# Kernel tuning notes

Hardware: AMD Instinct MI355X
Metric: run time of the kernel (lower is better)

## Reference

```python
import jax, jax.numpy as jnp
import numpy as np

B, S, D, H, F = 16, 512, 1024, 16, 4096
DH = D // H
LN_EPS = 1e-12


def layer_norm(x, g, b):
    mu = jnp.mean(x, axis=-1, keepdims=True)
    var = jnp.mean(jnp.square(x - mu), axis=-1, keepdims=True)
    return (x - mu) * jax.lax.rsqrt(var + LN_EPS) * g + b


def setup_inputs() -> dict:
    key = jax.random.key(0)
    ks = jax.random.split(key, 16)
    s_attn = 1.0 / np.sqrt(D)
    s_ffn = 1.0 / np.sqrt(F)
    return {
        "hidden_states": jax.random.normal(ks[0], (B, S, D), jnp.float32),
        "attention_mask": jnp.zeros((B, S), jnp.float32),
        # weights stored [in, out]
        "Wq": jax.random.normal(ks[1], (D, D), jnp.float32) * s_attn,
        "bq": jnp.zeros((D,), jnp.float32),
        "Wk": jax.random.normal(ks[2], (D, D), jnp.float32) * s_attn,
        "bk": jnp.zeros((D,), jnp.float32),
        "Wv": jax.random.normal(ks[3], (D, D), jnp.float32) * s_attn,
        "bv": jnp.zeros((D,), jnp.float32),
        "Wo": jax.random.normal(ks[4], (D, D), jnp.float32) * s_attn,
        "bo": jnp.zeros((D,), jnp.float32),
        "ln1_g": jnp.ones((D,), jnp.float32),
        "ln1_b": jnp.zeros((D,), jnp.float32),
        "Wi": jax.random.normal(ks[5], (D, F), jnp.float32) * s_attn,
        "bi": jnp.zeros((F,), jnp.float32),
        "Wo2": jax.random.normal(ks[6], (F, D), jnp.float32) * s_ffn,
        "bo2": jnp.zeros((D,), jnp.float32),
        "ln2_g": jnp.ones((D,), jnp.float32),
        "ln2_b": jnp.zeros((D,), jnp.float32),
    }


def reference(hidden_states, attention_mask, Wq, bq, Wk, bk, Wv, bv, Wo, bo,
              ln1_g, ln1_b, Wi, bi, Wo2, bo2, ln2_g, ln2_b):
    x = hidden_states
    # --- self attention ---
    q = (x @ Wq + bq).reshape(B, S, H, DH)
    k = (x @ Wk + bk).reshape(B, S, H, DH)
    v = (x @ Wv + bv).reshape(B, S, H, DH)
    scores = jnp.einsum("bqhd,bkhd->bhqk", q, k) / np.sqrt(DH)
    scores = scores + attention_mask[:, None, None, :]
    probs = jax.nn.softmax(scores, axis=-1)  # dropout p=0 (eval)
    ctx = jnp.einsum("bhqk,bkhd->bqhd", probs, v).reshape(B, S, D)
    # --- self output: dense + residual + LN ---
    attn_out = layer_norm(ctx @ Wo + bo + x, ln1_g, ln1_b)
    # --- intermediate: dense + gelu (exact erf gelu, BERT) ---
    inter = jax.nn.gelu(attn_out @ Wi + bi, approximate=False)
    # --- output: dense + residual + LN ---
    out = layer_norm(inter @ Wo2 + bo2 + attn_out, ln2_g, ln2_b)
    return out
```

## Files before the change

kernel.cpp:

```cpp
#include <hip/hip_runtime.h>
#include <hip/hip_bf16.h>
#include <math.h>

#define DEV_INLINE __device__ __forceinline__

typedef __attribute__((ext_vector_type(8))) short bf16x8;
typedef __attribute__((ext_vector_type(8))) unsigned short u16x8;
typedef __attribute__((ext_vector_type(4))) float f32x4;


DEV_INLINE void gload_lds16(const void* g, void* l) {
  __builtin_amdgcn_global_load_lds(
      (__attribute__((address_space(1))) unsigned int*)const_cast<void*>(g),
      (__attribute__((address_space(3))) unsigned int*)l,
      16, 0, 0);
}

DEV_INLINE unsigned lds_a(const void* p) {
  return (unsigned)(unsigned long long)(__attribute__((address_space(3))) const void*)p;
}

DEV_INLINE short f2bs(float x) {
  union { __hip_bfloat16 h; short s; } u;
  u.h = __float2bfloat16(x);
  return u.s;
}

DEV_INLINE float bs2f(unsigned short s) {
  union { float f; unsigned u; } v;
  v.u = ((unsigned)s) << 16;
  return v.f;
}

DEV_INLINE f32x4 mfma16(bf16x8 a, bf16x8 b, f32x4 c) {
  return __builtin_amdgcn_mfma_f32_16x16x32_bf16(a, b, c, 0, 0, 0);
}

#define DSREAD_O(dst, base, imm) \
  asm volatile("ds_read_b128 %0, %1 offset:%2" : "=v"(dst) : "v"(base), "n"(imm))


__global__ __launch_bounds__(256)
void prep_all(const float* __restrict__ X, __hip_bfloat16* __restrict__ Xb,
              const float* __restrict__ Wq, const float* __restrict__ Wk,
              const float* __restrict__ Wv, const float* __restrict__ Wo,
              const float* __restrict__ Wi, const float* __restrict__ Wo2,
              __hip_bfloat16* __restrict__ WqkvT, __hip_bfloat16* __restrict__ WoT,
              __hip_bfloat16* __restrict__ WiT, __hip_bfloat16* __restrict__ Wo2T,
              const float* __restrict__ bq, const float* __restrict__ bk,
              const float* __restrict__ bv, float* __restrict__ bqkv)
{
  int bx = blockIdx.x;
  const int tid = threadIdx.x;

  if (bx < 8192) {
    const size_t i = ((size_t)bx * 256 + tid) * 4;
    const float4 x = *(const float4*)(X + i);
    union { __hip_bfloat16 h[4]; ushort4 u; } pk;
    pk.h[0] = __float2bfloat16(x.x);
    pk.h[1] = __float2bfloat16(x.y);
    pk.h[2] = __float2bfloat16(x.z);
    pk.h[3] = __float2bfloat16(x.w);
    *(ushort4*)(Xb + i) = pk.u;
    return;
  }
  bx -= 8192;
  if (bx < 4) {
    const int i = bx * 256 + tid;
    bqkv[i] = bq[i]; bqkv[1024 + i] = bk[i]; bqkv[2048 + i] = bv[i];
    return;
  }
  bx -= 4;

  const float* Wsrc; __hip_bfloat16* Wdst; int K, N, nt, kt;
  if (bx < 1024)      { Wsrc = Wq;  Wdst = WqkvT;               K = 1024; N = 1024; nt = bx & 31;  kt = bx >> 5; }
  else if (bx < 2048) { const int l = bx - 1024; Wsrc = Wk;  Wdst = WqkvT + 1024 * 1024; K = 1024; N = 1024; nt = l & 31;  kt = l >> 5; }
  else if (bx < 3072) { const int l = bx - 2048; Wsrc = Wv;  Wdst = WqkvT + 2048 * 1024; K = 1024; N = 1024; nt = l & 31;  kt = l >> 5; }
  else if (bx < 4096) { const int l = bx - 3072; Wsrc = Wo;  Wdst = WoT;  K = 1024; N = 1024; nt = l & 31;  kt = l >> 5; }
  else if (bx < 8192) { const int l = bx - 4096; Wsrc = Wi;  Wdst = WiT;  K = 1024; N = 4096; nt = l & 127; kt = l >> 7; }
  else                { const int l = bx - 8192; Wsrc = Wo2; Wdst = Wo2T; K = 4096; N = 1024; nt = l & 31;  kt = l >> 5; }

  __shared__ float t[32][33];
  const int n0 = nt * 32, k0 = kt * 32;
  const int tx = tid & 31, ty = tid >> 5;
#pragma unroll
  for (int r = ty; r < 32; r += 8)
    t[r][tx] = Wsrc[(size_t)(k0 + r) * N + n0 + tx];
  __syncthreads();
#pragma unroll
  for (int r = ty; r < 32; r += 8)
    Wdst[(size_t)(n0 + r) * K + k0 + tx] = __float2bfloat16(t[tx][r]);
}


template<int MODE>
DEV_INLINE void gemm256_body(const short* __restrict__ A, const short* __restrict__ Bt,
                             const float* __restrict__ bias,
                             __hip_bfloat16* __restrict__ Cb,
                             int M, int N, int K)
{
  __shared__ __align__(128) short lds[24576];

  const int tid = threadIdx.x;
  const int lane = tid & 63, wid = tid >> 6;
  const int q4 = lane >> 4, c16 = lane & 15;
  const int wm = (wid >> 1) * 64, wn = (wid & 1) * 64;

  const int nNT = N >> 7;
  int bid = blockIdx.x;
  { const int cpx = (int)gridDim.x >> 3; bid = (bid & 7) * cpx + (bid >> 3); }
  const int bm = (bid / nNT) * 256;
  const int bn = (bid % nNT) * 128;

  const int sr = tid >> 3, sl = tid & 7;
  const int sg = (sl ^ (sr & 7)) * 8;
  const short* pA = A  + (size_t)(bm + sr) * K + sg;
  const short* pB = Bt + (size_t)(bn + sr) * K + sg;
  char* const baseA = (char*)lds;
  char* const baseB = (char*)lds + 32768;

  f32x4 acc[4][4];
#pragma unroll
  for (int i = 0; i < 4; ++i)
#pragma unroll
    for (int j = 0; j < 4; ++j) acc[i][j] = (f32x4){0.f, 0.f, 0.f, 0.f};

  for (int kt = 0; kt < K; kt += 64) {
    __syncthreads();
#pragma unroll
    for (int u = 0; u < 4; ++u)
      gload_lds16(pA + (size_t)u * 64 * K + kt, baseA + u * 8192 + wid * 1024);
#pragma unroll
    for (int u = 0; u < 2; ++u)
      gload_lds16(pB + (size_t)u * 64 * K + kt, baseB + u * 8192 + wid * 1024);
    __syncthreads();

#pragma unroll
    for (int kk = 0; kk < 2; ++kk) {
      bf16x8 af[4], bfr[4];
#pragma unroll
      for (int mt = 0; mt < 4; ++mt)
        af[mt] = *(const bf16x8*)(baseA + (wm + mt * 16 + c16) * 128 +
                                  (((kk * 4 + q4) ^ (c16 & 7)) * 16));
#pragma unroll
      for (int nt = 0; nt < 4; ++nt)
        bfr[nt] = *(const bf16x8*)(baseB + (wn + nt * 16 + c16) * 128 +
                                   (((kk * 4 + q4) ^ (c16 & 7)) * 16));
#pragma unroll
      for (int mt = 0; mt < 4; ++mt)
#pragma unroll
        for (int nt = 0; nt < 4; ++nt)
          acc[mt][nt] = mfma16(af[mt], bfr[nt], acc[mt][nt]);
    }
  }

  __syncthreads();

  float* eb = (float*)((char*)lds + wid * 4352);
  const int erow = lane >> 2, ecol = (lane & 3) * 16;
#pragma unroll
  for (int mf = 0; mf < 4; ++mf) {
#pragma unroll
    for (int nf = 0; nf < 4; ++nf) {
      const int col = bn + wn + nf * 16 + c16;
      const float bsv = bias[col];
#pragma unroll
      for (int j = 0; j < 4; ++j) {
        float v = acc[mf][nf][j] + bsv;
        if constexpr (MODE == 2)
          v = 0.5f * v * (1.0f + erff(v * 0.70710678118654752f));
        eb[(q4 * 4 + j) * 68 + nf * 16 + c16] = v;
      }
    }
    const int gr = bm + wm + mf * 16 + erow;
    const size_t gbase = (size_t)gr * N + bn + wn + ecol;
    unsigned short* cp = (unsigned short*)Cb;
#pragma unroll
    for (int u = 0; u < 2; ++u) {
      float4 a = *(float4*)&eb[erow * 68 + ecol + u * 8];
      float4 b = *(float4*)&eb[erow * 68 + ecol + u * 8 + 4];
      u16x8 o;
      o[0] = (unsigned short)f2bs(a.x); o[1] = (unsigned short)f2bs(a.y);
      o[2] = (unsigned short)f2bs(a.z); o[3] = (unsigned short)f2bs(a.w);
      o[4] = (unsigned short)f2bs(b.x); o[5] = (unsigned short)f2bs(b.y);
      o[6] = (unsigned short)f2bs(b.z); o[7] = (unsigned short)f2bs(b.w);
      *(u16x8*)(cp + gbase + u * 8) = o;
    }
  }
}


template<int MODE>
DEV_INLINE void gemm64_body(const short* __restrict__ A, const short* __restrict__ Bt,
                            const float* __restrict__ bias,
                            const float* __restrict__ residf,
                            const unsigned short* __restrict__ residb,
                            __hip_bfloat16* __restrict__ Cb,
                            int M, int N, int K)
{
  __shared__ __align__(128) short lds[32768];

  const int tid = threadIdx.x;
  const int lane = tid & 63, w = tid >> 6;
  const int q4 = lane >> 4, c16 = lane & 15;
  const int wm = (w >> 1) * 64, wn = (w & 1) * 64;

  const int nNT = N >> 7;
  int bid = blockIdx.x;
  { const int cpx = (int)gridDim.x >> 3; bid = (bid & 7) * cpx + (bid >> 3); }
  const int bm = (bid / nNT) * 128;
  const int bn = (bid % nNT) * 128;

  const int sr = tid >> 3, sl = tid & 7;
  const int sg = (sl ^ (sr & 7)) * 8;
  const short* pA = A  + (size_t)(bm + sr) * K + sg;
  const short* pB = Bt + (size_t)(bn + sr) * K + sg;

  const int s0 = (q4 ^ (c16 & 7)) * 16;
  const int s1 = ((q4 ^ 4) ^ (c16 & 7)) * 16;
  unsigned aRd0 = lds_a(lds) + (unsigned)((wm + c16) * 128 + s0);
  unsigned aRd1 = lds_a(lds) + (unsigned)((wm + c16) * 128 + s1);
  unsigned bRd0 = lds_a(lds) + (unsigned)(16384 + (wn + c16) * 128 + s0);
  unsigned bRd1 = lds_a(lds) + (unsigned)(16384 + (wn + c16) * 128 + s1);

  f32x4 acc[4][4];
#pragma unroll
  for (int i = 0; i < 4; ++i)
#pragma unroll
    for (int j = 0; j < 4; ++j) acc[i][j] = (f32x4){0.f, 0.f, 0.f, 0.f};

  auto stage = [&](int buf, int kt) {
    char* b = (char*)lds + buf * 32768;
#pragma unroll
    for (int u = 0; u < 4; ++u) {
      gload_lds16(pA + (size_t)u * 32 * K + kt, b + u * 4096 + w * 1024);
      gload_lds16(pB + (size_t)u * 32 * K + kt, b + 16384 + u * 4096 + w * 1024);
    }
  };

  stage(0, 0);
  __syncthreads();

  const int NT = K >> 6;
  int cur = 0;
  for (int t = 0; t < NT; ++t) {
    __builtin_amdgcn_sched_barrier(0);
    if (t + 1 < NT) stage(cur ^ 1, (t + 1) << 6);
    __builtin_amdgcn_sched_barrier(0);

    bf16x8 a0, a1, a2, a3, a4, a5, a6, a7;
    bf16x8 b0, b1, b2, b3, b4, b5, b6, b7;
    DSREAD_O(a0, aRd0, 0 * 2048); DSREAD_O(a1, aRd0, 1 * 2048);
    DSREAD_O(a2, aRd0, 2 * 2048); DSREAD_O(a3, aRd0, 3 * 2048);
    DSREAD_O(b0, bRd0, 0 * 2048); DSREAD_O(b1, bRd0, 1 * 2048);
    DSREAD_O(b2, bRd0, 2 * 2048); DSREAD_O(b3, bRd0, 3 * 2048);
    DSREAD_O(a4, aRd1, 0 * 2048); DSREAD_O(a5, aRd1, 1 * 2048);
    DSREAD_O(a6, aRd1, 2 * 2048); DSREAD_O(a7, aRd1, 3 * 2048);
    DSREAD_O(b4, bRd1, 0 * 2048); DSREAD_O(b5, bRd1, 1 * 2048);
    DSREAD_O(b6, bRd1, 2 * 2048); DSREAD_O(b7, bRd1, 3 * 2048);

    asm volatile("s_waitcnt lgkmcnt(0)");
    __builtin_amdgcn_sched_barrier(0);
    __builtin_amdgcn_s_setprio(1);
    acc[0][0] = mfma16(a0, b0, acc[0][0]); acc[0][1] = mfma16(a0, b1, acc[0][1]);
    acc[0][2] = mfma16(a0, b2, acc[0][2]); acc[0][3] = mfma16(a0, b3, acc[0][3]);
    acc[1][0] = mfma16(a1, b0, acc[1][0]); acc[1][1] = mfma16(a1, b1, acc[1][1]);
    acc[1][2] = mfma16(a1, b2, acc[1][2]); acc[1][3] = mfma16(a1, b3, acc[1][3]);
    acc[2][0] = mfma16(a2, b0, acc[2][0]); acc[2][1] = mfma16(a2, b1, acc[2][1]);
    acc[2][2] = mfma16(a2, b2, acc[2][2]); acc[2][3] = mfma16(a2, b3, acc[2][3]);
    acc[3][0] = mfma16(a3, b0, acc[3][0]); acc[3][1] = mfma16(a3, b1, acc[3][1]);
    acc[3][2] = mfma16(a3, b2, acc[3][2]); acc[3][3] = mfma16(a3, b3, acc[3][3]);
    acc[0][0] = mfma16(a4, b4, acc[0][0]); acc[0][1] = mfma16(a4, b5, acc[0][1]);
    acc[0][2] = mfma16(a4, b6, acc[0][2]); acc[0][3] = mfma16(a4, b7, acc[0][3]);
    acc[1][0] = mfma16(a5, b4, acc[1][0]); acc[1][1] = mfma16(a5, b5, acc[1][1]);
    acc[1][2] = mfma16(a5, b6, acc[1][2]); acc[1][3] = mfma16(a5, b7, acc[1][3]);
    acc[2][0] = mfma16(a6, b4, acc[2][0]); acc[2][1] = mfma16(a6, b5, acc[2][1]);
    acc[2][2] = mfma16(a6, b6, acc[2][2]); acc[2][3] = mfma16(a6, b7, acc[2][3]);
    acc[3][0] = mfma16(a7, b4, acc[3][0]); acc[3][1] = mfma16(a7, b5, acc[3][1]);
    acc[3][2] = mfma16(a7, b6, acc[3][2]); acc[3][3] = mfma16(a7, b7, acc[3][3]);
    __builtin_amdgcn_s_setprio(0);

    __syncthreads();
    aRd0 ^= 0x8000; aRd1 ^= 0x8000; bRd0 ^= 0x8000; bRd1 ^= 0x8000; cur ^= 1;
  }

  float* eb = (float*)((char*)lds + w * 4352);
  const int erow = lane >> 2, ecol = (lane & 3) * 16;
#pragma unroll
  for (int mf = 0; mf < 4; ++mf) {
#pragma unroll
    for (int nf = 0; nf < 4; ++nf) {
      const int col = bn + wn + nf * 16 + c16;
      const float bsv = bias[col];
#pragma unroll
      for (int j = 0; j < 4; ++j)
        eb[(q4 * 4 + j) * 68 + nf * 16 + c16] = acc[mf][nf][j] + bsv;
    }
    const int gr = bm + wm + mf * 16 + erow;
    const size_t gbase = (size_t)gr * N + bn + wn + ecol;
    unsigned short* cp = (unsigned short*)Cb;
#pragma unroll
    for (int u = 0; u < 2; ++u) {
      float4 a = *(float4*)&eb[erow * 68 + ecol + u * 8];
      float4 b = *(float4*)&eb[erow * 68 + ecol + u * 8 + 4];
      if constexpr (MODE == 3) {
        const float4 ra = *(const float4*)&residf[gbase + u * 8];
        const float4 rb = *(const float4*)&residf[gbase + u * 8 + 4];
        a.x += ra.x; a.y += ra.y; a.z += ra.z; a.w += ra.w;
        b.x += rb.x; b.y += rb.y; b.z += rb.z; b.w += rb.w;
      } else {
        const u16x8 rv = *(const u16x8*)(residb + gbase + u * 8);
        a.x += bs2f(rv[0]); a.y += bs2f(rv[1]); a.z += bs2f(rv[2]); a.w += bs2f(rv[3]);
        b.x += bs2f(rv[4]); b.y += bs2f(rv[5]); b.z += bs2f(rv[6]); b.w += bs2f(rv[7]);
      }
      u16x8 o;
      o[0] = (unsigned short)f2bs(a.x); o[1] = (unsigned short)f2bs(a.y);
      o[2] = (unsigned short)f2bs(a.z); o[3] = (unsigned short)f2bs(a.w);
      o[4] = (unsigned short)f2bs(b.x); o[5] = (unsigned short)f2bs(b.y);
      o[6] = (unsigned short)f2bs(b.z); o[7] = (unsigned short)f2bs(b.w);
      *(u16x8*)(cp + gbase + u * 8) = o;
    }
  }
}

__global__ __launch_bounds__(512)
void gemm_qkv(const short* A, const short* Bt, const float* bias,
              __hip_bfloat16* Cb, int M, int N, int K) {
  gemm256_body<0>(A, Bt, bias, Cb, M, N, K);
}
__global__ __launch_bounds__(512)
void gemm_wi(const short* A, const short* Bt, const float* bias,
             __hip_bfloat16* Cb, int M, int N, int K) {
  gemm256_body<2>(A, Bt, bias, Cb, M, N, K);
}
__global__ __launch_bounds__(256)
void gemm_wo(const short* A, const short* Bt, const float* bias,
             const float* residf, __hip_bfloat16* Cb, int M, int N, int K) {
  gemm64_body<3>(A, Bt, bias, residf, nullptr, Cb, M, N, K);
}
__global__ __launch_bounds__(256)
void gemm_wo2(const short* A, const short* Bt, const float* bias,
              const unsigned short* residb, __hip_bfloat16* Cb, int M, int N, int K) {
  gemm64_body<4>(A, Bt, bias, nullptr, residb, Cb, M, N, K);
}


__global__ __launch_bounds__(256)
void attn_flash(const short* __restrict__ Q, const short* __restrict__ Kmat,
                const short* __restrict__ V, const float* __restrict__ mask,
                __hip_bfloat16* __restrict__ ctx, int qs)
{
  __shared__ short Ksm[64 * 64];
  __shared__ short Vsm[64 * 64];
  __shared__ short Psm[4 * 16 * 64];

  const int tid = threadIdx.x;
  const int lane = tid & 63;
  const int w = tid >> 6;
  const int q4 = lane >> 4;
  const int c16 = lane & 15;
  const int b = blockIdx.z;
  const int h = blockIdx.y;
  const int qb = blockIdx.x;

  const size_t rowbase = (size_t)b * 512;
  const int hoff = h * 64;

  bf16x8 aq[2];
  {
    const size_t qrow = rowbase + (size_t)qb * 64 + w * 16 + c16;
    const short* qp = Q + qrow * qs + hoff + q4 * 8;
    aq[0] = *(const bf16x8*)(qp);
    aq[1] = *(const bf16x8*)(qp + 32);
  }

  float m_r[4], l_r[4];
  f32x4 O[4];
#pragma unroll
  for (int j = 0; j < 4; ++j) { m_r[j] = -INFINITY; l_r[j] = 0.f; O[j] = (f32x4){0.f, 0.f, 0.f, 0.f}; }

  const int kc0 = w * 128 + lane;
  const int kp0 = kc0 >> 3, kd0 = (kc0 & 7) * 8;
  const int kc1 = kc0 + 64;
  const int kp1 = kc1 >> 3, kd1 = (kc1 & 7) * 8;

  for (int kv0 = 0; kv0 < 512; kv0 += 64) {
    __syncthreads();
    gload_lds16(Kmat + (rowbase + kv0 + kp0) * qs + hoff + (kd0 ^ ((kp0 & 7) << 3)),
                (char*)Ksm + (size_t)(w * 128 + 0) * 16);
    gload_lds16(Kmat + (rowbase + kv0 + kp1) * qs + hoff + (kd1 ^ ((kp1 & 7) << 3)),
                (char*)Ksm + (size_t)(w * 128 + 64) * 16);
#pragma unroll
    for (int it = 0; it < 2; ++it) {
      const int c = tid + 256 * it;
      const int kp = c >> 3;
      const int dh8 = (c & 7) * 8;
      const bf16x8 vv = *(const bf16x8*)(V + (rowbase + kv0 + kp) * qs + hoff + dh8);
#pragma unroll
      for (int j = 0; j < 8; ++j) {
        const int dh = dh8 + j;
        *(short*)((char*)Vsm + dh * 128 + ((kp * 2) ^ ((dh & 7) << 4))) = vv[j];
      }
    }
    __syncthreads();

    float pv[4][4];
    float mk[4];
#pragma unroll
    for (int t = 0; t < 4; ++t) mk[t] = mask[rowbase + kv0 + t * 16 + c16];
#pragma unroll
    for (int t = 0; t < 4; ++t) {
      f32x4 z = (f32x4){0.f, 0.f, 0.f, 0.f};
      const int kp = t * 16 + c16;
#pragma unroll
      for (int ks = 0; ks < 2; ++ks) {
        const int d = ks * 32 + q4 * 8;
        bf16x8 kf = *(const bf16x8*)((char*)Ksm + kp * 128 + ((d * 2) ^ ((kp & 7) << 4)));
        z = mfma16(aq[ks], kf, z);
      }
#pragma unroll
      for (int j = 0; j < 4; ++j) pv[t][j] = z[j] * 0.125f + mk[t];
    }

#pragma unroll
    for (int j = 0; j < 4; ++j) {
      float mt_ = fmaxf(fmaxf(pv[0][j], pv[1][j]), fmaxf(pv[2][j], pv[3][j]));
#pragma unroll
      for (int o = 8; o >= 1; o >>= 1) mt_ = fmaxf(mt_, __shfl_xor(mt_, o));
      const float mn = fmaxf(m_r[j], mt_);
      const float sc = __expf(m_r[j] - mn);
      float rs = 0.f;
#pragma unroll
      for (int t = 0; t < 4; ++t) { const float pe = __expf(pv[t][j] - mn); pv[t][j] = pe; rs += pe; }
#pragma unroll
      for (int o = 8; o >= 1; o >>= 1) rs += __shfl_xor(rs, o);
      l_r[j] = l_r[j] * sc + rs;
      m_r[j] = mn;
#pragma unroll
      for (int nt = 0; nt < 4; ++nt) O[nt][j] *= sc;
    }

    char* pb = (char*)Psm + w * 2048;
#pragma unroll
    for (int j = 0; j < 4; ++j) {
      const int r = q4 * 4 + j;
#pragma unroll
      for (int t = 0; t < 4; ++t) {
        const int ck = t * 16 + c16;
        *(short*)(pb + r * 128 + ((ck * 2) ^ ((r & 7) << 4))) = f2bs(pv[t][j]);
      }
    }

#pragma unroll
    for (int ks = 0; ks < 2; ++ks) {
      const int kk = ks * 32 + q4 * 8;
      bf16x8 pa = *(const bf16x8*)(pb + c16 * 128 + ((kk * 2) ^ ((c16 & 7) << 4)));
#pragma unroll
      for (int nt = 0; nt < 4; ++nt) {
        const int dh = nt * 16 + c16;
        bf16x8 vf = *(const bf16x8*)((char*)Vsm + dh * 128 + ((kk * 2) ^ ((dh & 7) << 4)));
        O[nt] = mfma16(pa, vf, O[nt]);
      }
    }
  }

  float rinv[4];
#pragma unroll
  for (int j = 0; j < 4; ++j) rinv[j] = 1.0f / l_r[j];
#pragma unroll
  for (int nt = 0; nt < 4; ++nt) {
#pragma unroll
    for (int j = 0; j < 4; ++j) {
      const size_t row = rowbase + (size_t)qb * 64 + w * 16 + q4 * 4 + j;
      ctx[row * 1024 + hoff + nt * 16 + c16] = __float2bfloat16(O[nt][j] * rinv[j]);
    }
  }
}


template<int OUTB>
DEV_INLINE void ln_body(const unsigned short* __restrict__ in, const float* __restrict__ gam,
                        const float* __restrict__ bet, float* __restrict__ outf,
                        unsigned short* __restrict__ outb)
{
  const int row = blockIdx.x;
  const int tid = threadIdx.x;
  const size_t base = (size_t)row * 1024 + tid * 4;
  const ushort4 xi = *(const ushort4*)(in + base);
  const float x0 = bs2f(xi.x), x1 = bs2f(xi.y), x2 = bs2f(xi.z), x3 = bs2f(xi.w);
  float s  = x0 + x1 + x2 + x3;
  float s2 = x0 * x0 + x1 * x1 + x2 * x2 + x3 * x3;
#pragma unroll
  for (int o = 32; o >= 1; o >>= 1) { s += __shfl_xor(s, o); s2 += __shfl_xor(s2, o); }
  __shared__ float sb[8];
  const int w = tid >> 6;
  if ((tid & 63) == 0) { sb[w] = s; sb[w + 4] = s2; }
  __syncthreads();
  const float ts  = sb[0] + sb[1] + sb[2] + sb[3];
  const float ts2 = sb[4] + sb[5] + sb[6] + sb[7];
  const float mu = ts * (1.0f / 1024.0f);
  const float var = ts2 * (1.0f / 1024.0f) - mu * mu;
  const float rstd = rsqrtf(var + 1e-12f);
  const float4 g4 = *(const float4*)(gam + tid * 4);
  const float4 b4 = *(const float4*)(bet + tid * 4);
  const float y0 = (x0 - mu) * rstd * g4.x + b4.x;
  const float y1 = (x1 - mu) * rstd * g4.y + b4.y;
  const float y2 = (x2 - mu) * rstd * g4.z + b4.z;
  const float y3 = (x3 - mu) * rstd * g4.w + b4.w;
  if constexpr (OUTB) {
    ushort4 o;
    o.x = (unsigned short)f2bs(y0); o.y = (unsigned short)f2bs(y1);
    o.z = (unsigned short)f2bs(y2); o.w = (unsigned short)f2bs(y3);
    *(ushort4*)(outb + base) = o;
  } else {
    float4 y; y.x = y0; y.y = y1; y.z = y2; y.w = y3;
    *(float4*)(outf + base) = y;
  }
}

__global__ __launch_bounds__(256)
void ln_attn(const unsigned short* in, const float* gam, const float* bet,
             unsigned short* outb) { ln_body<1>(in, gam, bet, nullptr, outb); }
__global__ __launch_bounds__(256)
void ln_ffn(const unsigned short* in, const float* gam, const float* bet, float* outf) {
  ln_body<0>(in, gam, bet, outf, nullptr);
}


extern "C" void kernel_launch(void* const* d_in, const int* in_sizes, int n_in,
                              void* d_out, int out_size, void* d_ws, size_t ws_size,
                              hipStream_t stream)
{
  const float* X    = (const float*)d_in[0];
  const float* mask = (const float*)d_in[1];
  const float* Wq   = (const float*)d_in[2];   const float* bq  = (const float*)d_in[3];
  const float* Wk   = (const float*)d_in[4];   const float* bk  = (const float*)d_in[5];
  const float* Wv   = (const float*)d_in[6];   const float* bv  = (const float*)d_in[7];
  const float* Wo   = (const float*)d_in[8];   const float* bo  = (const float*)d_in[9];
  const float* g1   = (const float*)d_in[10];  const float* b1  = (const float*)d_in[11];
  const float* Wi   = (const float*)d_in[12];  const float* bi  = (const float*)d_in[13];
  const float* Wo2  = (const float*)d_in[14];  const float* bo2 = (const float*)d_in[15];
  const float* g2   = (const float*)d_in[16];  const float* b2  = (const float*)d_in[17];
  float* out = (float*)d_out;
  (void)in_sizes; (void)n_in; (void)out_size; (void)ws_size;

  const size_t D = 1024, F = 4096;
  const size_t MN = 8192 * D;

  char* p = (char*)d_ws;
  auto alloc = [&](size_t bytes) { char* r = p; p += (bytes + 255) & ~(size_t)255; return r; };
  short* Xb    = (short*)alloc(MN * 2);
  short* QKVb  = (short*)alloc(8192 * 3072 * 2);
  short* WqkvT = (short*)alloc(3072 * D * 2);
  short* WoT   = (short*)alloc(D * D * 2);
  short* WiT   = (short*)alloc(D * F * 2);
  short* Wo2T  = (short*)alloc(D * F * 2);
  float* bqkv  = (float*)alloc(3072 * 4);
  short* I1    = (short*)alloc(8192 * F * 2);

  prep_all<<<dim3(20484), 256, 0, stream>>>(X, (__hip_bfloat16*)Xb,
                                            Wq, Wk, Wv, Wo, Wi, Wo2,
                                            (__hip_bfloat16*)WqkvT, (__hip_bfloat16*)WoT,
                                            (__hip_bfloat16*)WiT, (__hip_bfloat16*)Wo2T,
                                            bq, bk, bv, bqkv);

  gemm_qkv<<<dim3(768), 512, 0, stream>>>(Xb, WqkvT, bqkv, (__hip_bfloat16*)QKVb, 8192, 3072, 1024);

  attn_flash<<<dim3(8, 16, 16), 256, 0, stream>>>(QKVb, QKVb + 1024, QKVb + 2048, mask,
                                                  (__hip_bfloat16*)Xb, 3072);

  gemm_wo<<<dim3(512), 256, 0, stream>>>(Xb, WoT, bo, X, (__hip_bfloat16*)out, 8192, 1024, 1024);
  ln_attn<<<dim3(8192), 256, 0, stream>>>((const unsigned short*)out, g1, b1, (unsigned short*)QKVb);

  gemm_wi<<<dim3(1024), 512, 0, stream>>>(QKVb, WiT, bi, (__hip_bfloat16*)I1, 8192, 4096, 1024);

  gemm_wo2<<<dim3(512), 256, 0, stream>>>(I1, Wo2T, bo2, (const unsigned short*)QKVb,
                                          (__hip_bfloat16*)Xb, 8192, 1024, 4096);
  ln_ffn<<<dim3(8192), 256, 0, stream>>>((const unsigned short*)Xb, g2, b2, out);
}
```

Measured before the change: 359.2 us.

## Unify GEMMs into triple-buffered BK=32 pipeline with single barrier per step

Replaces the 256-row QKV/Wi GEMM kernel and the double-buffered 128x128 kernel with one 128x128 kernel. It uses three 32-wide K stages in 48KB of LDS, prefetches two steps ahead, and waits with vmcnt plus a single s_barrier per iteration. QKV and Wi now launch twice as many 256-thread blocks, and GELU moves into the shared epilogue. The aim is to hide global load latency better and fit more blocks per CU, at the cost of more loop iterations and fewer MFMAs per barrier.

```diff
diff --git a/kernel.cpp b/kernel.cpp
--- a/kernel.cpp
+++ b/kernel.cpp
@@ -94,111 +94,14 @@
 
 
 template<int MODE>
-DEV_INLINE void gemm256_body(const short* __restrict__ A, const short* __restrict__ Bt,
-                             const float* __restrict__ bias,
-                             __hip_bfloat16* __restrict__ Cb,
-                             int M, int N, int K)
-{
-  __shared__ __align__(128) short lds[24576];
-
-  const int tid = threadIdx.x;
-  const int lane = tid & 63, wid = tid >> 6;
-  const int q4 = lane >> 4, c16 = lane & 15;
-  const int wm = (wid >> 1) * 64, wn = (wid & 1) * 64;
-
-  const int nNT = N >> 7;
-  int bid = blockIdx.x;
-  { const int cpx = (int)gridDim.x >> 3; bid = (bid & 7) * cpx + (bid >> 3); }
-  const int bm = (bid / nNT) * 256;
-  const int bn = (bid % nNT) * 128;
-
-  const int sr = tid >> 3, sl = tid & 7;
-  const int sg = (sl ^ (sr & 7)) * 8;
-  const short* pA = A  + (size_t)(bm + sr) * K + sg;
-  const short* pB = Bt + (size_t)(bn + sr) * K + sg;
-  char* const baseA = (char*)lds;
-  char* const baseB = (char*)lds + 32768;
-
-  f32x4 acc[4][4];
-#pragma unroll
-  for (int i = 0; i < 4; ++i)
-#pragma unroll
-    for (int j = 0; j < 4; ++j) acc[i][j] = (f32x4){0.f, 0.f, 0.f, 0.f};
-
-  for (int kt = 0; kt < K; kt += 64) {
-    __syncthreads();
-#pragma unroll
-    for (int u = 0; u < 4; ++u)
-      gload_lds16(pA + (size_t)u * 64 * K + kt, baseA + u * 8192 + wid * 1024);
-#pragma unroll
-    for (int u = 0; u < 2; ++u)
-      gload_lds16(pB + (size_t)u * 64 * K + kt, baseB + u * 8192 + wid * 1024);
-    __syncthreads();
-
-#pragma unroll
-    for (int kk = 0; kk < 2; ++kk) {
-      bf16x8 af[4], bfr[4];
-#pragma unroll
-      for (int mt = 0; mt < 4; ++mt)
-        af[mt] = *(const bf16x8*)(baseA + (wm + mt * 16 + c16) * 128 +
-                                  (((kk * 4 + q4) ^ (c16 & 7)) * 16));
-#pragma unroll
-      for (int nt = 0; nt < 4; ++nt)
-        bfr[nt] = *(const bf16x8*)(baseB + (wn + nt * 16 + c16) * 128 +
-                                   (((kk * 4 + q4) ^ (c16 & 7)) * 16));
-#pragma unroll
-      for (int mt = 0; mt < 4; ++mt)
-#pragma unroll
-        for (int nt = 0; nt < 4; ++nt)
-          acc[mt][nt] = mfma16(af[mt], bfr[nt], acc[mt][nt]);
-    }
-  }
-
-  __syncthreads();
-
-  float* eb = (float*)((char*)lds + wid * 4352);
-  const int erow = lane >> 2, ecol = (lane & 3) * 16;
-#pragma unroll
-  for (int mf = 0; mf < 4; ++mf) {
-#pragma unroll
-    for (int nf = 0; nf < 4; ++nf) {
-      const int col = bn + wn + nf * 16 + c16;
-      const float bsv = bias[col];
-#pragma unroll
-      for (int j = 0; j < 4; ++j) {
-        float v = acc[mf][nf][j] + bsv;
-        if constexpr (MODE == 2)
-          v = 0.5f * v * (1.0f + erff(v * 0.70710678118654752f));
-        eb[(q4 * 4 + j) * 68 + nf * 16 + c16] = v;
-      }
-    }
-    const int gr = bm + wm + mf * 16 + erow;
-    const size_t gbase = (size_t)gr * N + bn + wn + ecol;
-    unsigned short* cp = (unsigned short*)Cb;
-#pragma unroll
-    for (int u = 0; u < 2; ++u) {
-      float4 a = *(float4*)&eb[erow * 68 + ecol + u * 8];
-      float4 b = *(float4*)&eb[erow * 68 + ecol + u * 8 + 4];
-      u16x8 o;
-      o[0] = (unsigned short)f2bs(a.x); o[1] = (unsigned short)f2bs(a.y);
-      o[2] = (unsigned short)f2bs(a.z); o[3] = (unsigned short)f2bs(a.w);
-      o[4] = (unsigned short)f2bs(b.x); o[5] = (unsigned short)f2bs(b.y);
-      o[6] = (unsigned short)f2bs(b.z); o[7] = (unsigned short)f2bs(b.w);
-      *(u16x8*)(cp + gbase + u * 8) = o;
-    }
-  }
-}
-
-
-template<int MODE>
-DEV_INLINE void gemm64_body(const short* __restrict__ A, const short* __restrict__ Bt,
+DEV_INLINE void gemmr3_body(const short* __restrict__ A, const short* __restrict__ Bt,
                             const float* __restrict__ bias,
                             const float* __restrict__ residf,
                             const unsigned short* __restrict__ residb,
                             __hip_bfloat16* __restrict__ Cb,
                             int M, int N, int K)
 {
-  __shared__ __align__(128) short lds[32768];
+  __shared__ __align__(128) short lds[24576];
 
   const int tid = threadIdx.x;
   const int lane = tid & 63, w = tid >> 6;
@@ -211,17 +114,15 @@
   const int bm = (bid / nNT) * 128;
   const int bn = (bid % nNT) * 128;
 
-  const int sr = tid >> 3, sl = tid & 7;
-  const int sg = (sl ^ (sr & 7)) * 8;
-  const short* pA = A  + (size_t)(bm + sr) * K + sg;
-  const short* pB = Bt + (size_t)(bn + sr) * K + sg;
-
-  const int s0 = (q4 ^ (c16 & 7)) * 16;
-  const int s1 = ((q4 ^ 4) ^ (c16 & 7)) * 16;
-  unsigned aRd0 = lds_a(lds) + (unsigned)((wm + c16) * 128 + s0);
-  unsigned aRd1 = lds_a(lds) + (unsigned)((wm + c16) * 128 + s1);
-  unsigned bRd0 = lds_a(lds) + (unsigned)(16384 + (wn + c16) * 128 + s0);
-  unsigned bRd1 = lds_a(lds) + (unsigned)(16384 + (wn + c16) * 128 + s1);
+  const int sr = tid >> 2, sl = tid & 3;
+  const int sg = (sl ^ (sr & 3)) * 8;
+  const short* pA0 = A  + (size_t)(bm + sr) * K + sg;
+  const short* pA1 = A  + (size_t)(bm + 64 + sr) * K + ((sl ^ ((sr + 64) & 3)) * 8);
+  const short* pB0 = Bt + (size_t)(bn + sr) * K + sg;
+  const short* pB1 = Bt + (size_t)(bn + 64 + sr) * K + ((sl ^ ((sr + 64) & 3)) * 8);
+
+  const unsigned aRd = lds_a(lds) + (unsigned)((wm + c16) * 64 + (q4 ^ (c16 & 3)) * 16);
+  const unsigned bRd = lds_a(lds) + (unsigned)(8192 + (wn + c16) * 64 + (q4 ^ (c16 & 3)) * 16);
 
   f32x4 acc[4][4];
 #pragma unroll
@@ -229,35 +130,33 @@
 #pragma unroll
     for (int j = 0; j < 4; ++j) acc[i][j] = (f32x4){0.f, 0.f, 0.f, 0.f};
 
-  auto stage = [&](int buf, int kt) {
-    char* b = (char*)lds + buf * 32768;
-#pragma unroll
-    for (int u = 0; u < 4; ++u) {
-      gload_lds16(pA + (size_t)u * 32 * K + kt, b + u * 4096 + w * 1024);
-      gload_lds16(pB + (size_t)u * 32 * K + kt, b + 16384 + u * 4096 + w * 1024);
-    }
+  auto stage = [&](unsigned off, int kt) {
+    char* b = (char*)lds + off;
+    gload_lds16(pA0 + kt, b + w * 1024);
+    gload_lds16(pA1 + kt, b + 4096 + w * 1024);
+    gload_lds16(pB0 + kt, b + 8192 + w * 1024);
+    gload_lds16(pB1 + kt, b + 12288 + w * 1024);
   };
 
   stage(0, 0);
-  __syncthreads();
-
-  const int NT = K >> 6;
-  int cur = 0;
+  stage(16384, 32);
+
+  const int NT = K >> 5;
+  unsigned off = 0, soff = 32768;
   for (int t = 0; t < NT; ++t) {
     __builtin_amdgcn_sched_barrier(0);
-    if (t + 1 < NT) stage(cur ^ 1, (t + 1) << 6);
+    if (t < NT - 1) { asm volatile("s_waitcnt vmcnt(4)"); }
+    else            { asm volatile("s_waitcnt vmcnt(0)"); }
+    asm volatile("s_barrier");
     __builtin_amdgcn_sched_barrier(0);
-
-    bf16x8 a0, a1, a2, a3, a4, a5, a6, a7;
-    bf16x8 b0, b1, b2, b3, b4, b5, b6, b7;
-    DSREAD_O(a0, aRd0, 0 * 2048); DSREAD_O(a1, aRd0, 1 * 2048);
-    DSREAD_O(a2, aRd0, 2 * 2048); DSREAD_O(a3, aRd0, 3 * 2048);
-    DSREAD_O(b0, bRd0, 0 * 2048); DSREAD_O(b1, bRd0, 1 * 2048);
-    DSREAD_O(b2, bRd0, 2 * 2048); DSREAD_O(b3, bRd0, 3 * 2048);
-    DSREAD_O(a4, aRd1, 0 * 2048); DSREAD_O(a5, aRd1, 1 * 2048);
-    DSREAD_O(a6, aRd1, 2 * 2048); DSREAD_O(a7, aRd1, 3 * 2048);
-    DSREAD_O(b4, bRd1, 0 * 2048); DSREAD_O(b5, bRd1, 1 * 2048);
-    DSREAD_O(b6, bRd1, 2 * 2048); DSREAD_O(b7, bRd1, 3 * 2048);
+    if (t + 2 < NT) stage(soff, (t + 2) << 5);
+    __builtin_amdgcn_sched_barrier(0);
+
+    bf16x8 a0, a1, a2, a3, b0, b1, b2, b3;
+    DSREAD_O(a0, aRd + off, 0 * 1024); DSREAD_O(a1, aRd + off, 1 * 1024);
+    DSREAD_O(a2, aRd + off, 2 * 1024); DSREAD_O(a3, aRd + off, 3 * 1024);
+    DSREAD_O(b0, bRd + off, 0 * 1024); DSREAD_O(b1, bRd + off, 1 * 1024);
+    DSREAD_O(b2, bRd + off, 2 * 1024); DSREAD_O(b3, bRd + off, 3 * 1024);
 
     asm volatile("s_waitcnt lgkmcnt(0)");
     __builtin_amdgcn_sched_barrier(0);
@@ -270,19 +169,13 @@
     acc[2][2] = mfma16(a2, b2, acc[2][2]); acc[2][3] = mfma16(a2, b3, acc[2][3]);
     acc[3][0] = mfma16(a3, b0, acc[3][0]); acc[3][1] = mfma16(a3, b1, acc[3][1]);
     acc[3][2] = mfma16(a3, b2, acc[3][2]); acc[3][3] = mfma16(a3, b3, acc[3][3]);
-    acc[0][0] = mfma16(a4, b4, acc[0][0]); acc[0][1] = mfma16(a4, b5, acc[0][1]);
-    acc[0][2] = mfma16(a4, b6, acc[0][2]); acc[0][3] = mfma16(a4, b7, acc[0][3]);
-    acc[1][0] = mfma16(a5, b4, acc[1][0]); acc[1][1] = mfma16(a5, b5, acc[1][1]);
-    acc[1][2] = mfma16(a5, b6, acc[1][2]); acc[1][3] = mfma16(a5, b7, acc[1][3]);
-    acc[2][0] = mfma16(a6, b4, acc[2][0]); acc[2][1] = mfma16(a6, b5, acc[2][1]);
-    acc[2][2] = mfma16(a6, b6, acc[2][2]); acc[2][3] = mfma16(a6, b7, acc[2][3]);
-    acc[3][0] = mfma16(a7, b4, acc[3][0]); acc[3][1] = mfma16(a7, b5, acc[3][1]);
-    acc[3][2] = mfma16(a7, b6, acc[3][2]); acc[3][3] = mfma16(a7, b7, acc[3][3]);
     __builtin_amdgcn_s_setprio(0);
 
-    __syncthreads();
-    aRd0 ^= 0x8000; aRd1 ^= 0x8000; bRd0 ^= 0x8000; bRd1 ^= 0x8000; cur ^= 1;
-  }
+    off  = (off  == 32768) ? 0 : off  + 16384;
+    soff = (soff == 32768) ? 0 : soff + 16384;
+  }
+
+  __syncthreads();
 
   float* eb = (float*)((char*)lds + w * 4352);
   const int erow = lane >> 2, ecol = (lane & 3) * 16;
@@ -293,8 +186,12 @@
       const int col = bn + wn + nf * 16 + c16;
       const float bsv = bias[col];
 #pragma unroll
-      for (int j = 0; j < 4; ++j)
-        eb[(q4 * 4 + j) * 68 + nf * 16 + c16] = acc[mf][nf][j] + bsv;
+      for (int j = 0; j < 4; ++j) {
+        float v = acc[mf][nf][j] + bsv;
+        if constexpr (MODE == 2)
+          v = 0.5f * v * (1.0f + erff(v * 0.70710678118654752f));
+        eb[(q4 * 4 + j) * 68 + nf * 16 + c16] = v;
+      }
     }
     const int gr = bm + wm + mf * 16 + erow;
     const size_t gbase = (size_t)gr * N + bn + wn + ecol;
@@ -308,7 +205,7 @@
         const float4 rb = *(const float4*)&residf[gbase + u * 8 + 4];
         a.x += ra.x; a.y += ra.y; a.z += ra.z; a.w += ra.w;
         b.x += rb.x; b.y += rb.y; b.z += rb.z; b.w += rb.w;
-      } else {
+      } else if constexpr (MODE == 4) {
         const u16x8 rv = *(const u16x8*)(residb + gbase + u * 8);
         a.x += bs2f(rv[0]); a.y += bs2f(rv[1]); a.z += bs2f(rv[2]); a.w += bs2f(rv[3]);
         b.x += bs2f(rv[4]); b.y += bs2f(rv[5]); b.z += bs2f(rv[6]); b.w += bs2f(rv[7]);
@@ -323,25 +220,25 @@
   }
 }
 
-__global__ __launch_bounds__(512)
+__global__ __launch_bounds__(256)
 void gemm_qkv(const short* A, const short* Bt, const float* bias,
               __hip_bfloat16* Cb, int M, int N, int K) {
-  gemm256_body<0>(A, Bt, bias, Cb, M, N, K);
-}
-__global__ __launch_bounds__(512)
+  gemmr3_body<0>(A, Bt, bias, nullptr, nullptr, Cb, M, N, K);
+}
+__global__ __launch_bounds__(256)
 void gemm_wi(const short* A, const short* Bt, const float* bias,
              __hip_bfloat16* Cb, int M, int N, int K) {
-  gemm256_body<2>(A, Bt, bias, Cb, M, N, K);
+  gemmr3_body<2>(A, Bt, bias, nullptr, nullptr, Cb, M, N, K);
 }
 __global__ __launch_bounds__(256)
 void gemm_wo(const short* A, const short* Bt, const float* bias,
              const float* residf, __hip_bfloat16* Cb, int M, int N, int K) {
-  gemm64_body<3>(A, Bt, bias, residf, nullptr, Cb, M, N, K);
+  gemmr3_body<3>(A, Bt, bias, residf, nullptr, Cb, M, N, K);
 }
 __global__ __launch_bounds__(256)
 void gemm_wo2(const short* A, const short* Bt, const float* bias,
               const unsigned short* residb, __hip_bfloat16* Cb, int M, int N, int K) {
-  gemm64_body<4>(A, Bt, bias, nullptr, residb, Cb, M, N, K);
+  gemmr3_body<4>(A, Bt, bias, nullptr, residb, Cb, M, N, K);
 }
 
 
@@ -564,7 +461,7 @@
                                             (__hip_bfloat16*)WiT, (__hip_bfloat16*)Wo2T,
                                             bq, bk, bv, bqkv);
 
-  gemm_qkv<<<dim3(768), 512, 0, stream>>>(Xb, WqkvT, bqkv, (__hip_bfloat16*)QKVb, 8192, 3072, 1024);
+  gemm_qkv<<<dim3(1536), 256, 0, stream>>>(Xb, WqkvT, bqkv, (__hip_bfloat16*)QKVb, 8192, 3072, 1024);
 
   attn_flash<<<dim3(8, 16, 16), 256, 0, stream>>>(QKVb, QKVb + 1024, QKVb + 2048, mask,
                                                   (__hip_bfloat16*)Xb, 3072);
@@ -572,7 +469,7 @@
   gemm_wo<<<dim3(512), 256, 0, stream>>>(Xb, WoT, bo, X, (__hip_bfloat16*)out, 8192, 1024, 1024);
   ln_attn<<<dim3(8192), 256, 0, stream>>>((const unsigned short*)out, g1, b1, (unsigned short*)QKVb);
 
-  gemm_wi<<<dim3(1024), 512, 0, stream>>>(QKVb, WiT, bi, (__hip_bfloat16*)I1, 8192, 4096, 1024);
+  gemm_wi<<<dim3(2048), 256, 0, stream>>>(QKVb, WiT, bi, (__hip_bfloat16*)I1, 8192, 4096, 1024);
 
   gemm_wo2<<<dim3(512), 256, 0, stream>>>(I1, Wo2T, bo2, (const unsigned short*)QKVb,
                                           (__hip_bfloat16*)Xb, 8192, 1024, 4096);
```

Result: slower. 398.8 us (+11.0%).
